# Optimization experiments

Measured on AMD Instinct MI355X. Metric: run time of the kernel, lower is better.

## Reference

```python
import jax, jax.numpy as jnp
import numpy as np

NUM_HEADS = 4


def _mha_pool(seg):
    """seg: [n_seg, S, H]. First 4 channels are attention logits (softmax over S),
    rest are values split into 4 heads; returns [n_seg, H-4]."""
    n_seg, S, H = seg.shape
    attn = jax.nn.softmax(seg[:, :, :NUM_HEADS], axis=1)          # [n, S, 4]
    vals = seg[:, :, NUM_HEADS:].reshape(n_seg, S, NUM_HEADS, -1)  # [n, S, 4, hd]
    pooled = jnp.einsum('nsh,nshd->nhd', attn, vals)               # [n, 4, hd]
    return pooled.reshape(n_seg, -1)


def setup_inputs() -> dict:
    key = jax.random.key(0)
    k1, k2, k3, k4 = jax.random.split(key, 4)
    T, D, H = 131072, 2048, 260
    embeddings = jax.random.normal(k1, (T, D), dtype=jnp.float32)
    labels = jax.random.randint(k2, (T,), 0, 2, dtype=jnp.int32)
    W_down = jax.random.normal(k3, (D, H), dtype=jnp.float32) / np.sqrt(D)
    b_down = jnp.zeros((H,), dtype=jnp.float32)
    W_final = jax.random.normal(k4, (H - NUM_HEADS, 1), dtype=jnp.float32) / np.sqrt(H - NUM_HEADS)
    b_final = jnp.zeros((1,), dtype=jnp.float32)
    return {
        'embeddings': embeddings,
        'W_down': W_down,
        'b_down': b_down,
        'W_final': W_final,
        'b_final': b_final,
        'labels': labels,
        'tokens_per_problem': 512,
        'tokens_per_line': 16,
    }


def reference(embeddings, W_down, b_down, W_final, b_final, labels,
              tokens_per_problem, tokens_per_line):
    T, D = embeddings.shape
    H = W_down.shape[1]
    # Dropout is identity in eval mode (reference baseline).
    proj = embeddings @ W_down + b_down                      # [T, H]
    # MHA_POOL_4_HEADS: keep attention logits raw, GELU (exact erf) the values.
    act = jnp.concatenate(
        [proj[:, :NUM_HEADS], jax.nn.gelu(proj[:, NUM_HEADS:], approximate=False)],
        axis=1)                                              # [T, H]

    P = T // tokens_per_problem
    problem_feat = _mha_pool(act.reshape(P, tokens_per_problem, H))   # [P, H-4]
    problem_logits = (problem_feat @ W_final + b_final)[:, 0]

    L = T // tokens_per_line
    line_feat = _mha_pool(act.reshape(L, tokens_per_line, H))         # [L, H-4]
    line_logits = (line_feat @ W_final + b_final)[:, 0]

    token_logits = (act[:, NUM_HEADS:] @ W_final + b_final)[:, 0]     # [T]

    problem_labels = labels.reshape(P, tokens_per_problem).min(axis=1)
    line_labels = labels.reshape(L, tokens_per_line).min(axis=1)
    return token_logits, line_logits, line_labels, problem_logits, problem_labels
```

## Files before the change

### kernel.cpp

```cpp
#include <hip/hip_runtime.h>
#include <hip/hip_bf16.h>
#include <math.h>

#define T_TOK   131072
#define D_IN    2048
#define H_CH    260
#define NFRAG   17
#define KSTEPS  64
#define STEP_BYTES  (NFRAG * 64 * 16)
#define CHUNK_BYTES (2 * STEP_BYTES)
#define NCHUNK  32

typedef __attribute__((ext_vector_type(8))) short bf16x8;
typedef __attribute__((ext_vector_type(4))) float f32x4;

__device__ inline short f2bf(float x) {
    __hip_bfloat16 h = __float2bfloat16(x);
    return __builtin_bit_cast(short, h);
}

__global__ void prep_wfrag(const float* __restrict__ W, __hip_bfloat16* __restrict__ Wf) {
    int g = blockIdx.x;
    int s = g / NFRAG, f = g % NFRAG;
    int lane = threadIdx.x;
    int k0 = s * 32 + (lane >> 4) * 8;
    int col = f * 16 + (lane & 15);
    short vals8[8];
#pragma unroll
    for (int j = 0; j < 8; j++) {
        float v = (col < H_CH) ? W[(size_t)(k0 + j) * H_CH + col] : 0.f;
        vals8[j] = f2bf(v);
    }
    *reinterpret_cast<bf16x8*>(reinterpret_cast<short*>(Wf) + ((size_t)g * 64 + lane) * 8) =
        *reinterpret_cast<bf16x8*>(vals8);
}

__global__ __launch_bounds__(512, 4)
void gemm_act(const float* __restrict__ emb, const __hip_bfloat16* __restrict__ Wfrag,
              const float* __restrict__ b_down, const float* __restrict__ W_final,
              const float* __restrict__ b_final,
              float* __restrict__ attnL, __hip_bfloat16* __restrict__ vals,
              float* __restrict__ token_logits) {
    __shared__ __align__(16) char smem[2 * CHUNK_BYTES];

    int wave = threadIdx.x >> 6;
    int lane = threadIdx.x & 63;
    int r0 = blockIdx.x * 128 + wave * 16;
    int row_in = lane & 15;
    int kbase = (lane >> 4) * 8;

    const char* gW = (const char*)Wfrag;

    auto stage_chunk = [&](int c, char* lbase) {
        const char* src = gW + (size_t)c * CHUNK_BYTES;
#pragma unroll
        for (int r = 0; r < 4; ++r) {
            int off = (r * 8 + wave) * 1024;
            __builtin_amdgcn_global_load_lds(
                (const __attribute__((address_space(1))) unsigned int*)(src + off + lane * 16),
                (__attribute__((address_space(3))) unsigned int*)(lbase + off), 16, 0, 0);
        }
        if (wave < 2) {
            int off = (32 + wave) * 1024;
            __builtin_amdgcn_global_load_lds(
                (const __attribute__((address_space(1))) unsigned int*)(src + off + lane * 16),
                (__attribute__((address_space(3))) unsigned int*)(lbase + off), 16, 0, 0);
        }
    };

    f32x4 acc[NFRAG];
#pragma unroll
    for (int f = 0; f < NFRAG; f++) acc[f] = (f32x4){0.f, 0.f, 0.f, 0.f};

    const float* aptr = emb + (size_t)(r0 + row_in) * D_IN + kbase;

    stage_chunk(0, smem);
    f32x4 cl = *reinterpret_cast<const f32x4*>(aptr);
    f32x4 ch = *reinterpret_cast<const f32x4*>(aptr + 4);
    f32x4 nl, nh;
    __syncthreads();

#define DO_STEP(AL, AH, BOFF)                                                     \
    {                                                                             \
        bf16x8 af;                                                                \
        af[0] = f2bf(AL[0]); af[1] = f2bf(AL[1]);                                 \
        af[2] = f2bf(AL[2]); af[3] = f2bf(AL[3]);                                 \
        af[4] = f2bf(AH[0]); af[5] = f2bf(AH[1]);                                 \
        af[6] = f2bf(AH[2]); af[7] = f2bf(AH[3]);                                 \
        const char* bb = smem + (BOFF) + lane * 16;                               \
        _Pragma("unroll")                                                         \
        for (int f = 0; f < NFRAG; f++) {                                         \
            bf16x8 bfr = *reinterpret_cast<const bf16x8*>(bb + f * 1024);         \
            acc[f] = __builtin_amdgcn_mfma_f32_16x16x32_bf16(af, bfr, acc[f], 0, 0, 0); \
        }                                                                         \
    }

    for (int c = 0; c < NCHUNK; ++c) {
        int base = (c & 1) * CHUNK_BYTES;
        if (c + 1 < NCHUNK) stage_chunk(c + 1, smem + ((c + 1) & 1) * CHUNK_BYTES);

        int off1 = (2 * c + 1) * 32;
        nl = *reinterpret_cast<const f32x4*>(aptr + off1);
        nh = *reinterpret_cast<const f32x4*>(aptr + off1 + 4);
        DO_STEP(cl, ch, base)

        int s2 = 2 * c + 2;
        int off2 = (s2 < KSTEPS ? s2 : 0) * 32;
        cl = *reinterpret_cast<const f32x4*>(aptr + off2);
        ch = *reinterpret_cast<const f32x4*>(aptr + off2 + 4);
        DO_STEP(nl, nh, base + STEP_BYTES)

        __syncthreads();
    }
#undef DO_STEP

    int colbase = lane & 15;
    int rgroup = (lane >> 4) * 4;
    float tp[4] = {0.f, 0.f, 0.f, 0.f};
#pragma unroll
    for (int f = 0; f < NFRAG; f++) {
        int n = f * 16 + colbase;
        float bias = (n < H_CH) ? b_down[n] : 0.f;
        float wf = (n >= 4 && n < H_CH) ? W_final[n - 4] : 0.f;
#pragma unroll
        for (int i = 0; i < 4; i++) {
            int row = r0 + rgroup + i;
            float v = acc[f][i] + bias;
            float a = (n < 4) ? v : 0.5f * v * (1.f + erff(v * 0.70710678118f));
            if (n < 4) {
                attnL[(size_t)row * 4 + n] = v;
            } else if (n < H_CH) {
                vals[(size_t)row * 256 + (n - 4)] = __float2bfloat16(a);
            }
            tp[i] += a * wf;
        }
    }
#pragma unroll
    for (int i = 0; i < 4; i++) {
        float v = tp[i];
        v += __shfl_xor(v, 1);
        v += __shfl_xor(v, 2);
        v += __shfl_xor(v, 4);
        v += __shfl_xor(v, 8);
        if ((lane & 15) == 0) token_logits[r0 + rgroup + i] = v + b_final[0];
    }
}

__global__ __launch_bounds__(256)
void pool_problem(const float* __restrict__ attnL, const __hip_bfloat16* __restrict__ vals,
                  const int* __restrict__ labels,
                  const float* __restrict__ W_final, const float* __restrict__ b_final,
                  float* __restrict__ out_logits, float* __restrict__ out_labels) {
    __shared__ float w_lds[512 * 4];
    __shared__ float wred[4][4];
    __shared__ float psum[4];
    __shared__ int   lred[4];

    int p = blockIdx.x;
    int t = threadIdx.x;
    int lane = t & 63, wid = t >> 6;
    const float* abase = attnL + (size_t)p * 512 * 4;

    f32x4 v0 = *reinterpret_cast<const f32x4*>(abase + (size_t)t * 4);
    f32x4 v1 = *reinterpret_cast<const f32x4*>(abase + (size_t)(t + 256) * 4);

    float mh[4];
#pragma unroll
    for (int h = 0; h < 4; h++) mh[h] = fmaxf(v0[h], v1[h]);
#pragma unroll
    for (int h = 0; h < 4; h++)
        for (int mask = 1; mask < 64; mask <<= 1) mh[h] = fmaxf(mh[h], __shfl_xor(mh[h], mask));
    if (lane == 0) {
#pragma unroll
        for (int h = 0; h < 4; h++) wred[wid][h] = mh[h];
    }
    __syncthreads();
#pragma unroll
    for (int h = 0; h < 4; h++)
        mh[h] = fmaxf(fmaxf(wred[0][h], wred[1][h]), fmaxf(wred[2][h], wred[3][h]));
    __syncthreads();

    float Zh[4];
    f32x4 e0, e1;
#pragma unroll
    for (int h = 0; h < 4; h++) {
        e0[h] = __expf(v0[h] - mh[h]);
        e1[h] = __expf(v1[h] - mh[h]);
        Zh[h] = e0[h] + e1[h];
    }
    *reinterpret_cast<f32x4*>(&w_lds[t * 4]) = e0;
    *reinterpret_cast<f32x4*>(&w_lds[(t + 256) * 4]) = e1;
#pragma unroll
    for (int h = 0; h < 4; h++)
        for (int mask = 1; mask < 64; mask <<= 1) Zh[h] += __shfl_xor(Zh[h], mask);
    if (lane == 0) {
#pragma unroll
        for (int h = 0; h < 4; h++) wred[wid][h] = Zh[h];
    }
    __syncthreads();
#pragma unroll
    for (int h = 0; h < 4; h++) Zh[h] = wred[0][h] + wred[1][h] + wred[2][h] + wred[3][h];

    int h = t >> 6;
    const __hip_bfloat16* col = vals + (size_t)p * 512 * 256 + t;
    float pooled = 0.f;
#pragma unroll 8
    for (int s = 0; s < 512; s++)
        pooled += w_lds[s * 4 + h] * __bfloat162float(col[(size_t)s * 256]);
    float part = (pooled / Zh[h]) * W_final[t];
    for (int mask = 1; mask < 64; mask <<= 1) part += __shfl_xor(part, mask);
    if (lane == 0) psum[wid] = part;

    int lmin = min(labels[p * 512 + t], labels[p * 512 + t + 256]);
    for (int mask = 1; mask < 64; mask <<= 1) lmin = min(lmin, __shfl_xor(lmin, mask));
    if (lane == 0) lred[wid] = lmin;
    __syncthreads();
    if (t == 0) {
        out_logits[p] = psum[0] + psum[1] + psum[2] + psum[3] + b_final[0];
        out_labels[p] = (float)min(min(lred[0], lred[1]), min(lred[2], lred[3]));
    }
}

__global__ __launch_bounds__(256)
void pool_line(const float* __restrict__ attnL, const __hip_bfloat16* __restrict__ vals,
               const int* __restrict__ labels,
               const float* __restrict__ W_final, const float* __restrict__ b_final,
               float* __restrict__ out_logits, float* __restrict__ out_labels) {
    int wid = threadIdx.x >> 6, lane = threadIdx.x & 63;
    int line = blockIdx.x * 4 + wid;

    float x = attnL[(size_t)line * 64 + lane];
    float mm = x;
    mm = fmaxf(mm, __shfl_xor(mm, 4));
    mm = fmaxf(mm, __shfl_xor(mm, 8));
    mm = fmaxf(mm, __shfl_xor(mm, 16));
    mm = fmaxf(mm, __shfl_xor(mm, 32));
    float e = __expf(x - mm);
    float Z = e;
    Z += __shfl_xor(Z, 4);
    Z += __shfl_xor(Z, 8);
    Z += __shfl_xor(Z, 16);
    Z += __shfl_xor(Z, 32);
    float w = e / Z;

    const __hip_bfloat16* vbase = vals + (size_t)line * 16 * 256;
    float logit_part = 0.f;
#pragma unroll
    for (int j = 0; j < 4; j++) {
        float pooled = 0.f;
#pragma unroll
        for (int s = 0; s < 16; s++) {
            float ws = __shfl(w, s * 4 + j);
            pooled += ws * __bfloat162float(vbase[(size_t)s * 256 + j * 64 + lane]);
        }
        logit_part += pooled * W_final[j * 64 + lane];
    }
    for (int mask = 1; mask < 64; mask <<= 1) logit_part += __shfl_xor(logit_part, mask);

    int lab = (lane < 16) ? labels[line * 16 + lane] : 0x7fffffff;
    for (int mask = 1; mask < 64; mask <<= 1) lab = min(lab, __shfl_xor(lab, mask));

    if (lane == 0) {
        out_logits[line] = logit_part + b_final[0];
        out_labels[line] = (float)lab;
    }
}

extern "C" void kernel_launch(void* const* d_in, const int* in_sizes, int n_in,
                              void* d_out, int out_size, void* d_ws, size_t ws_size,
                              hipStream_t stream) {
    const float* emb     = (const float*)d_in[0];
    const float* W_down  = (const float*)d_in[1];
    const float* b_down  = (const float*)d_in[2];
    const float* W_final = (const float*)d_in[3];
    const float* b_final = (const float*)d_in[4];
    const int*   labels  = (const int*)d_in[5];

    float* out      = (float*)d_out;
    float* tok      = out;
    float* line_lg  = out + 131072;
    float* line_lb  = out + 139264;
    float* prob_lg  = out + 147456;
    float* prob_lb  = out + 147712;

    __hip_bfloat16* Wfrag = (__hip_bfloat16*)d_ws;
    float* attnL = (float*)((char*)d_ws + ((size_t)4 << 20));
    __hip_bfloat16* vals = (__hip_bfloat16*)((char*)d_ws + ((size_t)8 << 20));

    prep_wfrag<<<KSTEPS * NFRAG, 64, 0, stream>>>(W_down, Wfrag);
    gemm_act<<<T_TOK / 128, 512, 0, stream>>>(emb, Wfrag, b_down, W_final, b_final,
                                              attnL, vals, tok);
    pool_problem<<<256, 256, 0, stream>>>(attnL, vals, labels, W_final, b_final, prob_lg, prob_lb);
    pool_line<<<2048, 256, 0, stream>>>(attnL, vals, labels, W_final, b_final, line_lg, line_lb);
}
```

Measured before the change: 352.8 us.

## Fold W_final into GEMM epilogue as per-head token scores, drop value tensor

The GEMM epilogue now computes, for each token, four per-head dot products of the GELU values with W_final and stores them as a small fp32 tensor, instead of writing the full bf16 value matrix. The problem and line pooling kernels then apply the softmax weights to these per-head scalars, using linearity of the pooled-feature times W_final product. This removes the large intermediate write and its two re-reads by the pooling kernels. The cost is extra selects and shuffle reductions in the epilogue and a change in summation order.

```diff
diff --git a/kernel.cpp b/kernel.cpp
--- a/kernel.cpp
+++ b/kernel.cpp
@@ -39,7 +39,7 @@
 void gemm_act(const float* __restrict__ emb, const __hip_bfloat16* __restrict__ Wfrag,
               const float* __restrict__ b_down, const float* __restrict__ W_final,
               const float* __restrict__ b_final,
-              float* __restrict__ attnL, __hip_bfloat16* __restrict__ vals,
+              float* __restrict__ attnL, float* __restrict__ uvals,
               float* __restrict__ token_logits) {
     __shared__ __align__(16) char smem[2 * CHUNK_BYTES];
 
@@ -116,120 +116,134 @@
 
     int colbase = lane & 15;
     int rgroup = (lane >> 4) * 4;
-    float tp[4] = {0.f, 0.f, 0.f, 0.f};
+    float tph[4][4];
+#pragma unroll
+    for (int i = 0; i < 4; i++)
+#pragma unroll
+        for (int h = 0; h < 4; h++) tph[i][h] = 0.f;
+
 #pragma unroll
     for (int f = 0; f < NFRAG; f++) {
         int n = f * 16 + colbase;
         float bias = (n < H_CH) ? b_down[n] : 0.f;
         float wf = (n >= 4 && n < H_CH) ? W_final[n - 4] : 0.f;
+        int hidx = (n >= 4) ? ((n - 4) >> 6) : 0;
 #pragma unroll
         for (int i = 0; i < 4; i++) {
             int row = r0 + rgroup + i;
             float v = acc[f][i] + bias;
             float a = (n < 4) ? v : 0.5f * v * (1.f + erff(v * 0.70710678118f));
-            if (n < 4) {
-                attnL[(size_t)row * 4 + n] = v;
-            } else if (n < H_CH) {
-                vals[(size_t)row * 256 + (n - 4)] = __float2bfloat16(a);
-            }
-            tp[i] += a * wf;
-        }
-    }
-#pragma unroll
-    for (int i = 0; i < 4; i++) {
-        float v = tp[i];
-        v += __shfl_xor(v, 1);
-        v += __shfl_xor(v, 2);
-        v += __shfl_xor(v, 4);
-        v += __shfl_xor(v, 8);
-        if ((lane & 15) == 0) token_logits[r0 + rgroup + i] = v + b_final[0];
+            if (n < 4) attnL[(size_t)row * 4 + n] = v;
+            float contrib = a * wf;
+            tph[i][0] += (hidx == 0) ? contrib : 0.f;
+            tph[i][1] += (hidx == 1) ? contrib : 0.f;
+            tph[i][2] += (hidx == 2) ? contrib : 0.f;
+            tph[i][3] += (hidx == 3) ? contrib : 0.f;
+        }
+    }
+#pragma unroll
+    for (int i = 0; i < 4; i++)
+#pragma unroll
+        for (int h = 0; h < 4; h++) {
+            float v = tph[i][h];
+            v += __shfl_xor(v, 1);
+            v += __shfl_xor(v, 2);
+            v += __shfl_xor(v, 4);
+            v += __shfl_xor(v, 8);
+            tph[i][h] = v;
+        }
+    if ((lane & 15) == 0) {
+#pragma unroll
+        for (int i = 0; i < 4; i++) {
+            int row = r0 + rgroup + i;
+            f32x4 u = (f32x4){tph[i][0], tph[i][1], tph[i][2], tph[i][3]};
+            *reinterpret_cast<f32x4*>(uvals + (size_t)row * 4) = u;
+            token_logits[row] = u[0] + u[1] + u[2] + u[3] + b_final[0];
+        }
     }
 }
 
 __global__ __launch_bounds__(256)
-void pool_problem(const float* __restrict__ attnL, const __hip_bfloat16* __restrict__ vals,
-                  const int* __restrict__ labels,
-                  const float* __restrict__ W_final, const float* __restrict__ b_final,
+void pool_problem(const float* __restrict__ attnL, const float* __restrict__ uvals,
+                  const int* __restrict__ labels, const float* __restrict__ b_final,
                   float* __restrict__ out_logits, float* __restrict__ out_labels) {
-    __shared__ float w_lds[512 * 4];
-    __shared__ float wred[4][4];
-    __shared__ float psum[4];
+    __shared__ float mred[4][4];
+    __shared__ float nred[4][4];
+    __shared__ float dred[4][4];
     __shared__ int   lred[4];
 
     int p = blockIdx.x;
     int t = threadIdx.x;
     int lane = t & 63, wid = t >> 6;
-    const float* abase = attnL + (size_t)p * 512 * 4;
-
-    f32x4 v0 = *reinterpret_cast<const f32x4*>(abase + (size_t)t * 4);
-    f32x4 v1 = *reinterpret_cast<const f32x4*>(abase + (size_t)(t + 256) * 4);
+    const float* ab = attnL + (size_t)p * 2048;
+    const float* ub = uvals + (size_t)p * 2048;
+
+    f32x4 x0 = *reinterpret_cast<const f32x4*>(ab + (size_t)t * 4);
+    f32x4 x1 = *reinterpret_cast<const f32x4*>(ab + (size_t)(t + 256) * 4);
+    f32x4 q0 = *reinterpret_cast<const f32x4*>(ub + (size_t)t * 4);
+    f32x4 q1 = *reinterpret_cast<const f32x4*>(ub + (size_t)(t + 256) * 4);
 
     float mh[4];
 #pragma unroll
-    for (int h = 0; h < 4; h++) mh[h] = fmaxf(v0[h], v1[h]);
+    for (int h = 0; h < 4; h++) mh[h] = fmaxf(x0[h], x1[h]);
 #pragma unroll
     for (int h = 0; h < 4; h++)
         for (int mask = 1; mask < 64; mask <<= 1) mh[h] = fmaxf(mh[h], __shfl_xor(mh[h], mask));
     if (lane == 0) {
 #pragma unroll
-        for (int h = 0; h < 4; h++) wred[wid][h] = mh[h];
+        for (int h = 0; h < 4; h++) mred[wid][h] = mh[h];
     }
     __syncthreads();
 #pragma unroll
     for (int h = 0; h < 4; h++)
-        mh[h] = fmaxf(fmaxf(wred[0][h], wred[1][h]), fmaxf(wred[2][h], wred[3][h]));
-    __syncthreads();
-
-    float Zh[4];
-    f32x4 e0, e1;
+        mh[h] = fmaxf(fmaxf(mred[0][h], mred[1][h]), fmaxf(mred[2][h], mred[3][h]));
+
+    float nh[4], dh[4];
 #pragma unroll
     for (int h = 0; h < 4; h++) {
-        e0[h] = __expf(v0[h] - mh[h]);
-        e1[h] = __expf(v1[h] - mh[h]);
-        Zh[h] = e0[h] + e1[h];
-    }
-    *reinterpret_cast<f32x4*>(&w_lds[t * 4]) = e0;
-    *reinterpret_cast<f32x4*>(&w_lds[(t + 256) * 4]) = e1;
+        float e0 = __expf(x0[h] - mh[h]);
+        float e1 = __expf(x1[h] - mh[h]);
+        dh[h] = e0 + e1;
+        nh[h] = e0 * q0[h] + e1 * q1[h];
+    }
 #pragma unroll
     for (int h = 0; h < 4; h++)
-        for (int mask = 1; mask < 64; mask <<= 1) Zh[h] += __shfl_xor(Zh[h], mask);
+        for (int mask = 1; mask < 64; mask <<= 1) {
+            nh[h] += __shfl_xor(nh[h], mask);
+            dh[h] += __shfl_xor(dh[h], mask);
+        }
     if (lane == 0) {
 #pragma unroll
-        for (int h = 0; h < 4; h++) wred[wid][h] = Zh[h];
-    }
-    __syncthreads();
-#pragma unroll
-    for (int h = 0; h < 4; h++) Zh[h] = wred[0][h] + wred[1][h] + wred[2][h] + wred[3][h];
-
-    int h = t >> 6;
-    const __hip_bfloat16* col = vals + (size_t)p * 512 * 256 + t;
-    float pooled = 0.f;
-#pragma unroll 8
-    for (int s = 0; s < 512; s++)
-        pooled += w_lds[s * 4 + h] * __bfloat162float(col[(size_t)s * 256]);
-    float part = (pooled / Zh[h]) * W_final[t];
-    for (int mask = 1; mask < 64; mask <<= 1) part += __shfl_xor(part, mask);
-    if (lane == 0) psum[wid] = part;
+        for (int h = 0; h < 4; h++) { nred[wid][h] = nh[h]; dred[wid][h] = dh[h]; }
+    }
 
     int lmin = min(labels[p * 512 + t], labels[p * 512 + t + 256]);
     for (int mask = 1; mask < 64; mask <<= 1) lmin = min(lmin, __shfl_xor(lmin, mask));
     if (lane == 0) lred[wid] = lmin;
     __syncthreads();
     if (t == 0) {
-        out_logits[p] = psum[0] + psum[1] + psum[2] + psum[3] + b_final[0];
+        float logit = b_final[0];
+#pragma unroll
+        for (int h = 0; h < 4; h++) {
+            float num = nred[0][h] + nred[1][h] + nred[2][h] + nred[3][h];
+            float den = dred[0][h] + dred[1][h] + dred[2][h] + dred[3][h];
+            logit += num / den;
+        }
+        out_logits[p] = logit;
         out_labels[p] = (float)min(min(lred[0], lred[1]), min(lred[2], lred[3]));
     }
 }
 
 __global__ __launch_bounds__(256)
-void pool_line(const float* __restrict__ attnL, const __hip_bfloat16* __restrict__ vals,
-               const int* __restrict__ labels,
-               const float* __restrict__ W_final, const float* __restrict__ b_final,
+void pool_line(const float* __restrict__ attnL, const float* __restrict__ uvals,
+               const int* __restrict__ labels, const float* __restrict__ b_final,
                float* __restrict__ out_logits, float* __restrict__ out_labels) {
     int wid = threadIdx.x >> 6, lane = threadIdx.x & 63;
     int line = blockIdx.x * 4 + wid;
 
     float x = attnL[(size_t)line * 64 + lane];
+    float u = uvals[(size_t)line * 64 + lane];
+
     float mm = x;
     mm = fmaxf(mm, __shfl_xor(mm, 4));
     mm = fmaxf(mm, __shfl_xor(mm, 8));
@@ -241,27 +255,15 @@
     Z += __shfl_xor(Z, 8);
     Z += __shfl_xor(Z, 16);
     Z += __shfl_xor(Z, 32);
-    float w = e / Z;
-
-    const __hip_bfloat16* vbase = vals + (size_t)line * 16 * 256;
-    float logit_part = 0.f;
-#pragma unroll
-    for (int j = 0; j < 4; j++) {
-        float pooled = 0.f;
-#pragma unroll
-        for (int s = 0; s < 16; s++) {
-            float ws = __shfl(w, s * 4 + j);
-            pooled += ws * __bfloat162float(vbase[(size_t)s * 256 + j * 64 + lane]);
-        }
-        logit_part += pooled * W_final[j * 64 + lane];
-    }
-    for (int mask = 1; mask < 64; mask <<= 1) logit_part += __shfl_xor(logit_part, mask);
+    float part = (e / Z) * u;
+
+    for (int mask = 1; mask < 64; mask <<= 1) part += __shfl_xor(part, mask);
 
     int lab = (lane < 16) ? labels[line * 16 + lane] : 0x7fffffff;
     for (int mask = 1; mask < 64; mask <<= 1) lab = min(lab, __shfl_xor(lab, mask));
 
     if (lane == 0) {
-        out_logits[line] = logit_part + b_final[0];
+        out_logits[line] = part + b_final[0];
         out_labels[line] = (float)lab;
     }
 }
@@ -285,11 +287,11 @@
 
     __hip_bfloat16* Wfrag = (__hip_bfloat16*)d_ws;
     float* attnL = (float*)((char*)d_ws + ((size_t)4 << 20));
-    __hip_bfloat16* vals = (__hip_bfloat16*)((char*)d_ws + ((size_t)8 << 20));
+    float* uvals = (float*)((char*)d_ws + ((size_t)8 << 20));
 
     prep_wfrag<<<KSTEPS * NFRAG, 64, 0, stream>>>(W_down, Wfrag);
     gemm_act<<<T_TOK / 128, 512, 0, stream>>>(emb, Wfrag, b_down, W_final, b_final,
-                                              attnL, vals, tok);
-    pool_problem<<<256, 256, 0, stream>>>(attnL, vals, labels, W_final, b_final, prob_lg, prob_lb);
-    pool_line<<<2048, 256, 0, stream>>>(attnL, vals, labels, W_final, b_final, line_lg, line_lb);
-}
+                                              attnL, uvals, tok);
+    pool_problem<<<256, 256, 0, stream>>>(attnL, uvals, labels, b_final, prob_lg, prob_lb);
+    pool_line<<<2048, 256, 0, stream>>>(attnL, uvals, labels, b_final, line_lg, line_lb);
+}
```

Result: slower. 398.3 us (+12.9%).
